# Kernel tuning notes

Hardware: AMD Instinct MI355X
Metric: run time of the kernel (lower is better)

Reference implementation:

```python
import jax, jax.numpy as jnp
import numpy as np
from jax import lax

# ---- static config (matches init_kwargs) ----
STRIDE = 16
BASE_SIZE = 16
SCALES = np.array([2., 4., 8., 16., 32.])
RATIOS = np.array([0.5, 1., 2.])
CLIP = 4.14
NMS_THRESH = 0.7
PRE_NMS = 6000
POST_NMS = 300
MIN_SIZE = 16.0


def _whctrs(a):
    w = a[2] - a[0] + 1.0
    h = a[3] - a[1] + 1.0
    return w, h, a[0] + 0.5 * (w - 1.0), a[1] + 0.5 * (h - 1.0)


def _mkanchors(ws, hs, xc, yc):
    return np.stack([xc - 0.5 * (ws - 1.0), yc - 0.5 * (hs - 1.0),
                     xc + 0.5 * (ws - 1.0), yc + 0.5 * (hs - 1.0)], axis=1)


def _base_anchors():
    ba = np.array([1.0, 1.0, BASE_SIZE, BASE_SIZE]) - 1.0
    w, h, xc, yc = _whctrs(ba)
    size = w * h
    ws = np.round(np.sqrt(size / RATIOS))
    hs = np.round(ws * RATIOS)
    ra = _mkanchors(ws, hs, xc, yc)
    out = []
    for i in range(ra.shape[0]):
        w, h, xc, yc = _whctrs(ra[i])
        out.append(_mkanchors(w * SCALES, h * SCALES, xc, yc))
    return np.concatenate(out, axis=0)  # (A,4), A = len(ratios)*len(scales)


def _grid_anchors(Hf, Wf):
    ba = _base_anchors()                       # (A,4)
    sx, sy = np.meshgrid(np.arange(Wf) * STRIDE, np.arange(Hf) * STRIDE)
    shifts = np.stack([sx, sy, sx, sy], axis=-1)          # (Hf,Wf,4)
    anch = shifts[:, :, None, :] + ba[None, None, :, :]    # (Hf,Wf,A,4)
    return jnp.asarray(anch.reshape(1, -1, 4), dtype=jnp.float32)


def _decode_clip(anchors, deltas, img_h, img_w):
    # NormalizedBoxCenterDecoder (stds=1) + clip to image
    aw = anchors[..., 2] - anchors[..., 0]
    ah = anchors[..., 3] - anchors[..., 1]
    ax = anchors[..., 0] + 0.5 * aw
    ay = anchors[..., 1] + 0.5 * ah
    dx, dy, dw, dh = deltas[..., 0], deltas[..., 1], deltas[..., 2], deltas[..., 3]
    ox = dx * aw + ax
    oy = dy * ah + ay
    ow = jnp.exp(jnp.minimum(dw, CLIP)) * aw * 0.5
    oh = jnp.exp(jnp.minimum(dh, CLIP)) * ah * 0.5
    x1 = jnp.clip(ox - ow, 0.0, img_w - 1.0)
    y1 = jnp.clip(oy - oh, 0.0, img_h - 1.0)
    x2 = jnp.clip(ox + ow, 0.0, img_w - 1.0)
    y2 = jnp.clip(oy + oh, 0.0, img_h - 1.0)
    return jnp.stack([x1, y1, x2, y2], axis=-1)


def _nms_single(scores, boxes):
    # scores (N,), boxes (N,4). Greedy NMS, force_suppress, sorted by score desc.
    order = jnp.argsort(-scores)[:PRE_NMS]
    s = scores[order]
    b = boxes[order]
    x1, y1, x2, y2 = b[:, 0], b[:, 1], b[:, 2], b[:, 3]
    area = (x2 - x1) * (y2 - y1)
    iw = jnp.maximum(jnp.minimum(x2[:, None], x2[None, :]) - jnp.maximum(x1[:, None], x1[None, :]), 0.0)
    ih = jnp.maximum(jnp.minimum(y2[:, None], y2[None, :]) - jnp.maximum(y1[:, None], y1[None, :]), 0.0)
    inter = iw * ih
    iou = inter / (area[:, None] + area[None, :] - inter + 1e-12)  # (PRE,PRE)

    supp0 = s < 0.0  # invalid entries (score set to -1 by min_size filter)

    def body(supp, i):
        keep = jnp.logical_not(supp[i])
        new = jnp.where(keep, jnp.logical_or(supp, iou[i] > NMS_THRESH), supp)
        new = new.at[i].set(supp[i])  # never self-suppress
        return new, None

    supp, _ = lax.scan(body, supp0, jnp.arange(PRE_NMS))
    kept = jnp.logical_not(supp)
    perm = jnp.argsort(jnp.where(kept, 0, 1), stable=True)  # kept boxes first, order preserved
    out_s = jnp.where(kept[perm], s[perm], -1.0)
    out_b = jnp.where(kept[perm][:, None], b[perm], -1.0)
    return out_s[:POST_NMS, None], out_b[:POST_NMS]


def _forward(img, x, conv_w, conv_b, score_w, score_b, loc_w, loc_b):
    B, _, Hf, Wf = x.shape
    img_h, img_w = float(img.shape[2]), float(img.shape[3])
    anchors = _grid_anchors(Hf, Wf)  # (1, Hf*Wf*A, 4)

    # conv1 3x3 pad 1 + ReLU
    h = lax.conv_general_dilated(x, conv_w, (1, 1), [(1, 1), (1, 1)],
                                 dimension_numbers=('NCHW', 'OIHW', 'NCHW'))
    h = jax.nn.relu(h + conv_b[None, :, None, None])

    A = score_w.shape[0]
    raw_scores = jnp.einsum('bchw,oc->bhwo', h, score_w.reshape(A, -1)) + score_b
    raw_scores = raw_scores.reshape(B, -1, 1)                       # (B,N,1)
    raw_boxes = jnp.einsum('bchw,oc->bhwo', h, loc_w.reshape(4 * A, -1)) + loc_b
    raw_boxes = raw_boxes.reshape(B, -1, 4)                         # (B,N,4)

    rpn_scores = jax.nn.sigmoid(raw_scores)

    roi = _decode_clip(anchors, raw_boxes, img_h, img_w)            # (B,N,4)
    width = roi[..., 2] - roi[..., 0]
    height = roi[..., 3] - roi[..., 1]
    invalid = jnp.logical_or(width < MIN_SIZE, height < MIN_SIZE)   # (B,N)
    score = jnp.where(invalid[..., None], -1.0, rpn_scores)         # (B,N,1)
    roi = jnp.where(invalid[..., None], -1.0, roi)

    out_s, out_b = jax.vmap(_nms_single)(score[..., 0], roi)        # (B,300,1),(B,300,4)
    return jnp.concatenate([out_s, out_b], axis=-1)                 # (B,300,5)


def setup_inputs() -> dict:
    key = jax.random.key(0)
    ks = jax.random.split(key, 8)
    img = jax.random.normal(ks[0], (1, 3, 1024, 1024), jnp.float32)
    x = jax.random.normal(ks[1], (1, 1024, 64, 64), jnp.float32)
    conv_w = jax.random.normal(ks[2], (1024, 1024, 3, 3), jnp.float32) * 0.01
    conv_b = jnp.zeros((1024,), jnp.float32)
    score_w = jax.random.normal(ks[3], (15, 1024, 1, 1), jnp.float32) * 0.01
    score_b = jnp.zeros((15,), jnp.float32)
    loc_w = jax.random.normal(ks[4], (60, 1024, 1, 1), jnp.float32) * 0.002
    loc_b = jnp.zeros((60,), jnp.float32)
    return {"img": img, "x": x, "conv_w": conv_w, "conv_b": conv_b,
            "score_w": score_w, "score_b": score_b, "loc_w": loc_w, "loc_b": loc_b}


def reference(img, x, conv_w, conv_b, score_w, score_b, loc_w, loc_b):
    return _forward(img, x, conv_w, conv_b, score_w, score_b, loc_w, loc_b)
```

## Files before the change

kernel.cpp:

```cpp
#include <hip/hip_runtime.h>

typedef unsigned int uint;
typedef unsigned short ushort;
typedef unsigned long long u64;

typedef __attribute__((ext_vector_type(8))) short short8;
typedef __attribute__((ext_vector_type(4))) float floatx4;

__device__ inline ushort bf16rne(float v) {
  uint b = __float_as_uint(v);
  uint r = (b + 0x7fffu + ((b >> 16) & 1u)) >> 16;
  return (ushort)r;
}

__device__ inline void gl_lds16(const void* g, void* l) {
  __builtin_amdgcn_global_load_lds(
      (const __attribute__((address_space(1))) unsigned int*)g,
      (__attribute__((address_space(3))) unsigned int*)l, 16, 0, 0);
}

__global__ __launch_bounds__(256) void prep_x(const float* __restrict__ x,
                                              ushort* __restrict__ xh,
                                              ushort* __restrict__ xl) {
  __shared__ float tile[64 * 65];
  int ci0 = blockIdx.x * 64, y = blockIdx.y, t = threadIdx.x;
#pragma unroll
  for (int it = 0; it < 16; ++it) {
    int L = t + 256 * it;
    int cl = L >> 6, xx = L & 63;
    tile[cl * 65 + xx] = x[(size_t)(ci0 + cl) * 4096 + y * 64 + xx];
  }
  __syncthreads();
#pragma unroll
  for (int it = 0; it < 16; ++it) {
    int L = t + 256 * it;
    int xx = L >> 6, cl = L & 63;
    float v = tile[cl * 65 + xx];
    ushort h2 = bf16rne(v);
    float hf = __uint_as_float((uint)h2 << 16);
    ushort l2 = bf16rne(v - hf);
    size_t oi = ((size_t)((y + 1) * 66 + (xx + 1))) * 1024 + ci0 + cl;
    xh[oi] = h2;
    xl[oi] = l2;
  }
}

__global__ __launch_bounds__(256) void prep_w(const float* __restrict__ w,
                                              ushort* __restrict__ wh,
                                              ushort* __restrict__ wl) {
  __shared__ float tile[2304];
  int co = blockIdx.x, ci0 = blockIdx.y * 256, t = threadIdx.x;
  const float* src = w + ((size_t)co * 1024 + ci0) * 9;
  for (int i = t; i < 2304; i += 256) tile[i] = src[i];
  __syncthreads();
  int ci = ci0 + t;
#pragma unroll
  for (int off = 0; off < 9; ++off) {
    float v = tile[t * 9 + off];
    ushort h2 = bf16rne(v);
    float hf = __uint_as_float((uint)h2 << 16);
    ushort l2 = bf16rne(v - hf);
    size_t oi = ((size_t)off << 20) | ((size_t)co << 10) | (size_t)ci;
    wh[oi] = h2;
    wl[oi] = l2;
  }
}

__global__ __launch_bounds__(256) void prep_head(
    const float* __restrict__ score_w, const float* __restrict__ loc_w,
    const float* __restrict__ score_b, const float* __restrict__ loc_b,
    ushort* __restrict__ wh, ushort* __restrict__ wl, float* __restrict__ bh) {
  int idx = blockIdx.x * 256 + threadIdx.x;
  int o = idx >> 10, ci = idx & 1023;
  float v = 0.f;
  if (o < 15) v = score_w[o * 1024 + ci];
  else if (o < 75) v = loc_w[(o - 15) * 1024 + ci];
  ushort h2 = bf16rne(v);
  float hf = __uint_as_float((uint)h2 << 16);
  wh[idx] = h2;
  wl[idx] = bf16rne(v - hf);
  if (idx < 128) bh[idx] = (idx < 15) ? score_b[idx] : ((idx < 75) ? loc_b[idx - 15] : 0.f);
}

template <int IM2COL>
__global__ __launch_bounds__(256, 1) void gemm_bf16x3(
    const ushort* __restrict__ Ahi, const ushort* __restrict__ Alo,
    const ushort* __restrict__ Bhi, const ushort* __restrict__ Blo,
    const float* __restrict__ bias, int nChunks, float* __restrict__ outRaw,
    ushort* __restrict__ outHi, ushort* __restrict__ outLo) {
  __shared__ ushort sm[2 * 4 * 128 * 32];
  const int t = threadIdx.x;
  const int m0 = blockIdx.x * 128;
  const int n0 = blockIdx.y * 128;

  auto stage = [&](int kc, int bufIdx) {
    char* lds = (char*)sm + bufIdx * 32768;
    int off = 0, cc = 0, oy = 0, ox = 0;
    if (IM2COL) {
      off = kc >> 5;
      cc = (kc & 31) << 5;
      oy = off / 3;
      ox = off - 3 * oy;
    }
#pragma unroll
    for (int q = 0; q < 2; ++q) {
      int L = t + 256 * q, row = L >> 2, seg = L & 3;
      size_t aoff, boff;
      if (IM2COL) {
        int m = m0 + row, y = m >> 6, xq = m & 63;
        aoff = ((size_t)((y + oy) * 66 + (xq + ox)) * 1024 + (size_t)cc) * 2 + seg * 16;
        boff = (((size_t)off << 20) + ((size_t)(n0 + row) << 10) + (size_t)cc) * 2 + seg * 16;
      } else {
        aoff = (((size_t)(m0 + row) << 10) + (size_t)kc * 32) * 2 + seg * 16;
        boff = (((size_t)(n0 + row) << 10) + (size_t)kc * 32) * 2 + seg * 16;
      }
      int dst = L * 16;
      gl_lds16((const char*)Ahi + aoff, lds + dst);
      gl_lds16((const char*)Alo + aoff, lds + 8192 + dst);
      gl_lds16((const char*)Bhi + boff, lds + 16384 + dst);
      gl_lds16((const char*)Blo + boff, lds + 24576 + dst);
    }
  };

  const int lane = t & 63, wv = t >> 6;
  const int wm = (wv & 1) * 64, wn = (wv >> 1) * 64;
  const int arow = wm + (lane & 15);
  const int brow = wn + (lane & 15);
  const int ko = (lane >> 4) * 8;

  floatx4 acc[4][4];
#pragma unroll
  for (int i = 0; i < 4; ++i)
#pragma unroll
    for (int j = 0; j < 4; ++j) acc[i][j] = (floatx4){0.f, 0.f, 0.f, 0.f};

  stage(0, 0);
  for (int kc = 0; kc < nChunks; ++kc) {
    __syncthreads();
    if (kc + 1 < nChunks) stage(kc + 1, (kc + 1) & 1);
    const ushort* sb = sm + (kc & 1) * 16384;
    const ushort* sAh = sb;
    const ushort* sAl = sb + 4096;
    const ushort* sBh = sb + 8192;
    const ushort* sBl = sb + 12288;
    short8 ah[4], al[4], bh2[4], bl2[4];
#pragma unroll
    for (int i = 0; i < 4; ++i) {
      ah[i] = *(const short8*)(sAh + (arow + 16 * i) * 32 + ko);
      al[i] = *(const short8*)(sAl + (arow + 16 * i) * 32 + ko);
      bh2[i] = *(const short8*)(sBh + (brow + 16 * i) * 32 + ko);
      bl2[i] = *(const short8*)(sBl + (brow + 16 * i) * 32 + ko);
    }
#pragma unroll
    for (int i = 0; i < 4; ++i)
#pragma unroll
      for (int j = 0; j < 4; ++j) {
        acc[i][j] = __builtin_amdgcn_mfma_f32_16x16x32_bf16(ah[i], bh2[j], acc[i][j], 0, 0, 0);
        acc[i][j] = __builtin_amdgcn_mfma_f32_16x16x32_bf16(ah[i], bl2[j], acc[i][j], 0, 0, 0);
        acc[i][j] = __builtin_amdgcn_mfma_f32_16x16x32_bf16(al[i], bh2[j], acc[i][j], 0, 0, 0);
      }
  }

#pragma unroll
  for (int i = 0; i < 4; ++i)
#pragma unroll
    for (int j = 0; j < 4; ++j) {
      int nn = n0 + wn + 16 * j + (lane & 15);
      float bv = bias[nn];
#pragma unroll
      for (int r = 0; r < 4; ++r) {
        int mm = m0 + wm + 16 * i + (lane >> 4) * 4 + r;
        float v = acc[i][j][r] + bv;
        if (IM2COL) {
          v = fmaxf(v, 0.f);
          ushort h2 = bf16rne(v);
          float hf = __uint_as_float((uint)h2 << 16);
          ushort l2 = bf16rne(v - hf);
          outHi[(size_t)mm * 1024 + nn] = h2;
          outLo[(size_t)mm * 1024 + nn] = l2;
        } else {
          outRaw[(size_t)mm * 128 + nn] = v;
        }
      }
    }
}

__global__ __launch_bounds__(256) void decode_k(const float* __restrict__ raw,
                                                float* __restrict__ scores,
                                                float4* __restrict__ boxes,
                                                uint* __restrict__ key32,
                                                uint* __restrict__ hist) {
  int i = blockIdx.x * 256 + threadIdx.x;
  int m = i / 15, a = i - m * 15;
  int y = m >> 6, x = m & 63;
  const float* rp = raw + (size_t)m * 128;
  float logit = rp[a];
  float dx = rp[15 + 4 * a], dy = rp[16 + 4 * a];
  float dw = rp[17 + 4 * a], dh = rp[18 + 4 * a];
  int rr = a / 5, ss = a - rr * 5;
  float sc5 = (float)(2 << ss);
  float W = ((rr == 0) ? 23.f : (rr == 1) ? 16.f : 11.f) * sc5;
  float H = ((rr == 0) ? 12.f : (rr == 1) ? 16.f : 22.f) * sc5;
  float aw = W - 1.f, ah = H - 1.f;
  float ax = x * 16.f + 7.5f, ay = y * 16.f + 7.5f;
  float ox = dx * aw + ax, oyc = dy * ah + ay;
  float ow = expf(fminf(dw, 4.14f)) * aw * 0.5f;
  float oh = expf(fminf(dh, 4.14f)) * ah * 0.5f;
  float x1 = fminf(fmaxf(ox - ow, 0.f), 1023.f);
  float y1 = fminf(fmaxf(oyc - oh, 0.f), 1023.f);
  float x2 = fminf(fmaxf(ox + ow, 0.f), 1023.f);
  float y2 = fminf(fmaxf(oyc + oh, 0.f), 1023.f);
  bool inval = ((x2 - x1) < 16.f) || ((y2 - y1) < 16.f);
  float sc = inval ? -1.f : (1.f / (1.f + expf(-logit)));
  scores[i] = sc;
  boxes[i] = inval ? make_float4(-1.f, -1.f, -1.f, -1.f) : make_float4(x1, y1, x2, y2);
  uint kb = __float_as_uint(sc);
  uint key = (kb & 0x80000000u) ? ~kb : (kb | 0x80000000u);
  key32[i] = key;
  atomicAdd(&hist[key >> 16], 1u);
}

__global__ __launch_bounds__(256) void find_t16(const uint* __restrict__ hist,
                                                uint* __restrict__ selT) {
  __shared__ uint ps[256];
  __shared__ int segS;
  int t = threadIdx.x;
  uint s = 0;
  const uint* hp = hist + t * 256;
  for (int i = 0; i < 256; ++i) s += hp[i];
  ps[t] = s;
  __syncthreads();
  for (int d = 1; d < 256; d <<= 1) {
    uint v = ps[t] + ((t + d < 256) ? ps[t + d] : 0u);
    __syncthreads();
    ps[t] = v;
    __syncthreads();
  }
  if (ps[t] >= 6000u && (t == 255 || ps[t + 1] < 6000u)) segS = t;
  __syncthreads();
  int sg = segS;
  uint base = (sg == 255) ? 0u : ps[sg + 1];
  uint h2 = hist[sg * 256 + t];
  __syncthreads();
  ps[t] = h2;
  __syncthreads();
  for (int d = 1; d < 256; d <<= 1) {
    uint v = ps[t] + ((t + d < 256) ? ps[t + d] : 0u);
    __syncthreads();
    ps[t] = v;
    __syncthreads();
  }
  if (base + ps[t] >= 6000u && (t == 255 || base + ps[t + 1] < 6000u))
    *selT = (uint)(sg * 256 + t);
}

__global__ __launch_bounds__(256) void gather_k(const uint* __restrict__ key32,
                                                const uint* __restrict__ selT,
                                                uint* __restrict__ cnt,
                                                u64* __restrict__ cand) {
  int i = blockIdx.x * 256 + threadIdx.x;
  uint T = *selT;
  uint k = key32[i];
  if ((k >> 16) >= T) {
    uint pos = atomicAdd(cnt, 1u);
    if (pos < 8192) cand[pos] = ((u64)k << 32) | (u64)(~(uint)i);
  }
}

__global__ __launch_bounds__(1024) void sort_gather(
    const u64* __restrict__ cand, const uint* __restrict__ cnt,
    const float* __restrict__ scores, const float4* __restrict__ boxes,
    float* __restrict__ sortedS, float4* __restrict__ sortedB) {
  extern __shared__ u64 sk[];
  int t = threadIdx.x;
  int C = (int)*cnt;
  if (C > 8192) C = 8192;
  for (int j = t; j < 8192; j += 1024) sk[j] = (j < C) ? cand[j] : 0ull;
  __syncthreads();
  for (int k = 2; k <= 8192; k <<= 1) {
    for (int j2 = k >> 1; j2 > 0; j2 >>= 1) {
      for (int p = t; p < 4096; p += 1024) {
        int i = ((p & ~(j2 - 1)) << 1) | (p & (j2 - 1));
        int ix = i | j2;
        u64 a = sk[i], b = sk[ix];
        bool ddir = (i & k) != 0;
        if ((a < b) != ddir) { sk[i] = b; sk[ix] = a; }
      }
      __syncthreads();
    }
  }
  for (int j = t; j < 6016; j += 1024) {
    if (j < 6000) {
      u64 key = sk[j];
      uint idx = ~(uint)(key & 0xffffffffu);
      sortedS[j] = scores[idx];
      sortedB[j] = boxes[idx];
    } else {
      sortedS[j] = -1.f;
      sortedB[j] = make_float4(0.f, 0.f, 0.f, 0.f);
    }
  }
}

__global__ __launch_bounds__(64) void iou_mask(const float4* __restrict__ boxes,
                                               u64* __restrict__ mask) {
  __shared__ float cx1[64], cy1[64], cx2[64], cy2[64], car[64];
  int bi = blockIdx.x, bj = blockIdx.y, t = threadIdx.x;
  float4 cb = boxes[bj * 64 + t];
  cx1[t] = cb.x; cy1[t] = cb.y; cx2[t] = cb.z; cy2[t] = cb.w;
  car[t] = (cb.z - cb.x) * (cb.w - cb.y);
  __syncthreads();
  int r = bi * 64 + t;
  float4 rb = boxes[r];
  float ra = (rb.z - rb.x) * (rb.w - rb.y);
  u64 wd = 0;
#pragma unroll 8
  for (int j = 0; j < 64; ++j) {
    float iw = fmaxf(fminf(rb.z, cx2[j]) - fmaxf(rb.x, cx1[j]), 0.f);
    float ih = fmaxf(fminf(rb.w, cy2[j]) - fmaxf(rb.y, cy1[j]), 0.f);
    float inter = iw * ih;
    float iou = inter / (ra + car[j] - inter + 1e-12f);
    if (iou > 0.7f && r != bj * 64 + j) wd |= (1ull << j);
  }
  mask[(size_t)r * 128 + bj] = wd;
}

__global__ __launch_bounds__(64) void nms_scan(const u64* __restrict__ mask,
                                               const float* __restrict__ sortedS,
                                               const float4* __restrict__ sortedB,
                                               float* __restrict__ out) {
  __shared__ int klist[300];
  int lane = threadIdx.x;
  u64 Sx = 0, Sy = 0;
  for (int w2 = 0; w2 < 94; ++w2) {
    bool neg = sortedS[w2 * 64 + lane] < 0.f;
    u64 m2 = __ballot(neg);
    if ((w2 >> 1) == lane) { if (w2 & 1) Sy = m2; else Sx = m2; }
  }
  int count = 0;
  for (int w2 = 0; w2 < 94; ++w2) {
    u64 cur = __shfl((w2 & 1) ? Sy : Sx, w2 >> 1);
    u64 rem = ~cur;
    if (w2 == 93) rem &= (1ull << 48) - 1;
    while (rem) {
      int b = __builtin_ctzll(rem);
      int i = w2 * 64 + b;
      if (lane == 0) klist[count] = i;
      count++;
      if (count == 300) goto done;
      const ulonglong2* rp = (const ulonglong2*)(mask + (size_t)i * 128);
      ulonglong2 rv = rp[lane];
      Sx |= rv.x;
      Sy |= rv.y;
      u64 cur2 = __shfl((w2 & 1) ? Sy : Sx, w2 >> 1);
      rem &= ~cur2;
      rem &= (b == 63) ? 0ull : (~0ull << (b + 1));
    }
  }
done:
  __syncthreads();
  for (int j = lane; j < 300; j += 64) {
    float s;
    float4 bb;
    if (j < count) {
      int i = klist[j];
      s = sortedS[i];
      bb = sortedB[i];
    } else {
      s = -1.f;
      bb = make_float4(-1.f, -1.f, -1.f, -1.f);
    }
    out[j * 5 + 0] = s;
    out[j * 5 + 1] = bb.x;
    out[j * 5 + 2] = bb.y;
    out[j * 5 + 3] = bb.z;
    out[j * 5 + 4] = bb.w;
  }
}

constexpr size_t O_XH = 0;
constexpr size_t O_XL = 8921088;
constexpr size_t O_WTH = 17842176;
constexpr size_t O_WTL = 36716544;
constexpr size_t O_HH = 55590912;
constexpr size_t O_HL = 63979520;
constexpr size_t O_WHH = 72368128;
constexpr size_t O_WHL = 72630272;
constexpr size_t O_BHD = 72892416;
constexpr size_t O_SC = 72892928;
constexpr size_t O_BX = 73138688;
constexpr size_t O_KEY = 74121728;
constexpr size_t O_HIST = 74367488;
constexpr size_t O_CNT = 74629632;
constexpr size_t O_CAND = 74629888;
constexpr size_t O_SELT = 74695424;
constexpr size_t O_SS = 74695680;
constexpr size_t O_SB = 74719744;
constexpr size_t O_RAW = 0;
constexpr size_t O_MASK = 17842176;

extern "C" void kernel_launch(void* const* d_in, const int* in_sizes, int n_in,
                              void* d_out, int out_size, void* d_ws,
                              size_t ws_size, hipStream_t stream) {
  (void)in_sizes; (void)n_in; (void)out_size; (void)ws_size;
  const float* x = (const float*)d_in[1];
  const float* conv_w = (const float*)d_in[2];
  const float* conv_b = (const float*)d_in[3];
  const float* score_w = (const float*)d_in[4];
  const float* score_b = (const float*)d_in[5];
  const float* loc_w = (const float*)d_in[6];
  const float* loc_b = (const float*)d_in[7];
  float* out = (float*)d_out;
  char* ws = (char*)d_ws;

  ushort* xh = (ushort*)(ws + O_XH);
  ushort* xl = (ushort*)(ws + O_XL);
  ushort* wTh = (ushort*)(ws + O_WTH);
  ushort* wTl = (ushort*)(ws + O_WTL);
  ushort* hh = (ushort*)(ws + O_HH);
  ushort* hl = (ushort*)(ws + O_HL);
  ushort* wHh = (ushort*)(ws + O_WHH);
  ushort* wHl = (ushort*)(ws + O_WHL);
  float* biasH = (float*)(ws + O_BHD);
  float* raw = (float*)(ws + O_RAW);
  float* scores = (float*)(ws + O_SC);
  float4* boxes = (float4*)(ws + O_BX);
  uint* key32 = (uint*)(ws + O_KEY);
  uint* hist = (uint*)(ws + O_HIST);
  uint* cnt = (uint*)(ws + O_CNT);
  u64* cand = (u64*)(ws + O_CAND);
  uint* selT = (uint*)(ws + O_SELT);
  float* sortedS = (float*)(ws + O_SS);
  float4* sortedB = (float4*)(ws + O_SB);
  u64* mask = (u64*)(ws + O_MASK);

  hipMemsetAsync(ws + O_XH, 0, 2 * 8921088, stream);
  hipMemsetAsync(ws + O_HIST, 0, 262144 + 256, stream);

  prep_x<<<dim3(16, 64), 256, 0, stream>>>(x, xh, xl);
  prep_w<<<dim3(1024, 4), 256, 0, stream>>>(conv_w, wTh, wTl);
  prep_head<<<512, 256, 0, stream>>>(score_w, loc_w, score_b, loc_b, wHh, wHl, biasH);

  gemm_bf16x3<1><<<dim3(32, 8), 256, 0, stream>>>(xh, xl, wTh, wTl, conv_b, 288,
                                                  nullptr, hh, hl);
  gemm_bf16x3<0><<<dim3(32, 1), 256, 0, stream>>>(hh, hl, wHh, wHl, biasH, 32,
                                                  raw, nullptr, nullptr);

  decode_k<<<240, 256, 0, stream>>>(raw, scores, boxes, key32, hist);
  find_t16<<<1, 256, 0, stream>>>(hist, selT);
  gather_k<<<240, 256, 0, stream>>>(key32, selT, cnt, cand);
  sort_gather<<<1, 1024, 65536, stream>>>(cand, cnt, scores, boxes, sortedS, sortedB);
  iou_mask<<<dim3(94, 94), 64, 0, stream>>>(sortedB, mask);
  nms_scan<<<1, 64, 0, stream>>>(mask, sortedS, sortedB, out);
}
```

Before: 744.1 us.

## Template GEMM on N tile width and switch LDS layout to segment-major

The bf16x3 GEMM is templated on the N tile size. The main 3x3 conv GEMM now uses 64-wide N tiles, giving 512 blocks instead of 256 so the mi355x's CUs are better filled. The LDS staging layout also changes from row-major (row, seg) to segment-major (seg, row), which changes the bank access pattern of the short8 fragment reads and likely reduces bank conflicts. Narrower tiles lower per-block arithmetic intensity and increase A-tile reloads from global memory.

```diff
diff --git a/kernel.cpp b/kernel.cpp
--- a/kernel.cpp
+++ b/kernel.cpp
@@ -82,79 +82,101 @@
   if (idx < 128) bh[idx] = (idx < 15) ? score_b[idx] : ((idx < 75) ? loc_b[idx - 15] : 0.f);
 }
 
-template <int IM2COL>
+template <int IM2COL, int BN>
 __global__ __launch_bounds__(256, 1) void gemm_bf16x3(
     const ushort* __restrict__ Ahi, const ushort* __restrict__ Alo,
     const ushort* __restrict__ Bhi, const ushort* __restrict__ Blo,
     const float* __restrict__ bias, int nChunks, float* __restrict__ outRaw,
     ushort* __restrict__ outHi, ushort* __restrict__ outLo) {
-  __shared__ ushort sm[2 * 4 * 128 * 32];
+  constexpr int ASEC = 128 * 32;
+  constexpr int BSEC = BN * 32;
+  constexpr int BUFU = 2 * ASEC + 2 * BSEC;
+  constexpr int NJ = BN / 32;
+  __shared__ ushort sm[2 * BUFU];
   const int t = threadIdx.x;
   const int m0 = blockIdx.x * 128;
-  const int n0 = blockIdx.y * 128;
-
-  auto stage = [&](int kc, int bufIdx) {
-    char* lds = (char*)sm + bufIdx * 32768;
+  const int n0 = blockIdx.y * BN;
+
+  auto stage = [&](int c, int bufIdx) {
+    ushort* secAh = sm + bufIdx * BUFU;
+    ushort* secAl = secAh + ASEC;
+    ushort* secBh = secAl + ASEC;
+    ushort* secBl = secBh + BSEC;
     int off = 0, cc = 0, oy = 0, ox = 0;
     if (IM2COL) {
-      off = kc >> 5;
-      cc = (kc & 31) << 5;
+      off = c >> 5;
+      cc = (c & 31) << 5;
       oy = off / 3;
       ox = off - 3 * oy;
     }
 #pragma unroll
     for (int q = 0; q < 2; ++q) {
-      int L = t + 256 * q, row = L >> 2, seg = L & 3;
-      size_t aoff, boff;
+      int L = t + 256 * q;
+      int row = L & 127, seg = L >> 7;
+      size_t aoff;
       if (IM2COL) {
         int m = m0 + row, y = m >> 6, xq = m & 63;
         aoff = ((size_t)((y + oy) * 66 + (xq + ox)) * 1024 + (size_t)cc) * 2 + seg * 16;
+      } else {
+        aoff = (((size_t)(m0 + row) << 10) + (size_t)c * 32) * 2 + seg * 16;
+      }
+      gl_lds16((const char*)Ahi + aoff, (char*)secAh + L * 16);
+      gl_lds16((const char*)Alo + aoff, (char*)secAl + L * 16);
+    }
+#pragma unroll
+    for (int q = 0; q < BN / 64; ++q) {
+      int L = t + 256 * q;
+      int row = L & (BN - 1), seg = L / BN;
+      size_t boff;
+      if (IM2COL) {
         boff = (((size_t)off << 20) + ((size_t)(n0 + row) << 10) + (size_t)cc) * 2 + seg * 16;
       } else {
-        aoff = (((size_t)(m0 + row) << 10) + (size_t)kc * 32) * 2 + seg * 16;
-        boff = (((size_t)(n0 + row) << 10) + (size_t)kc * 32) * 2 + seg * 16;
+        boff = (((size_t)(n0 + row) << 10) + (size_t)c * 32) * 2 + seg * 16;
       }
-      int dst = L * 16;
-      gl_lds16((const char*)Ahi + aoff, lds + dst);
-      gl_lds16((const char*)Alo + aoff, lds + 8192 + dst);
-      gl_lds16((const char*)Bhi + boff, lds + 16384 + dst);
-      gl_lds16((const char*)Blo + boff, lds + 24576 + dst);
+      gl_lds16((const char*)Bhi + boff, (char*)secBh + L * 16);
+      gl_lds16((const char*)Blo + boff, (char*)secBl + L * 16);
     }
   };
 
   const int lane = t & 63, wv = t >> 6;
-  const int wm = (wv & 1) * 64, wn = (wv >> 1) * 64;
-  const int arow = wm + (lane & 15);
-  const int brow = wn + (lane & 15);
-  const int ko = (lane >> 4) * 8;
-
-  floatx4 acc[4][4];
+  const int wm = (wv & 1) * 64, wn = (wv >> 1) * (BN / 2);
+  const int rA = wm + (lane & 15);
+  const int rB = wn + (lane & 15);
+  const int segA = (lane >> 4) * 2048;
+  const int segB = (lane >> 4) * (BN * 16);
+
+  floatx4 acc[4][NJ];
 #pragma unroll
   for (int i = 0; i < 4; ++i)
 #pragma unroll
-    for (int j = 0; j < 4; ++j) acc[i][j] = (floatx4){0.f, 0.f, 0.f, 0.f};
+    for (int j = 0; j < NJ; ++j) acc[i][j] = (floatx4){0.f, 0.f, 0.f, 0.f};
 
   stage(0, 0);
   for (int kc = 0; kc < nChunks; ++kc) {
     __syncthreads();
     if (kc + 1 < nChunks) stage(kc + 1, (kc + 1) & 1);
-    const ushort* sb = sm + (kc & 1) * 16384;
-    const ushort* sAh = sb;
-    const ushort* sAl = sb + 4096;
-    const ushort* sBh = sb + 8192;
-    const ushort* sBl = sb + 12288;
-    short8 ah[4], al[4], bh2[4], bl2[4];
+    const ushort* sb = sm + (kc & 1) * BUFU;
+    const char* cAh = (const char*)sb;
+    const char* cAl = (const char*)(sb + ASEC);
+    const char* cBh = (const char*)(sb + 2 * ASEC);
+    const char* cBl = (const char*)(sb + 2 * ASEC + BSEC);
+    short8 ah[4], al[4], bh2[NJ], bl2[NJ];
 #pragma unroll
     for (int i = 0; i < 4; ++i) {
-      ah[i] = *(const short8*)(sAh + (arow + 16 * i) * 32 + ko);
-      al[i] = *(const short8*)(sAl + (arow + 16 * i) * 32 + ko);
-      bh2[i] = *(const short8*)(sBh + (brow + 16 * i) * 32 + ko);
-      bl2[i] = *(const short8*)(sBl + (brow + 16 * i) * 32 + ko);
+      int pa = segA + (rA + 16 * i) * 16;
+      ah[i] = *(const short8*)(cAh + pa);
+      al[i] = *(const short8*)(cAl + pa);
+    }
+#pragma unroll
+    for (int j = 0; j < NJ; ++j) {
+      int pb = segB + (rB + 16 * j) * 16;
+      bh2[j] = *(const short8*)(cBh + pb);
+      bl2[j] = *(const short8*)(cBl + pb);
     }
 #pragma unroll
     for (int i = 0; i < 4; ++i)
 #pragma unroll
-      for (int j = 0; j < 4; ++j) {
+      for (int j = 0; j < NJ; ++j) {
         acc[i][j] = __builtin_amdgcn_mfma_f32_16x16x32_bf16(ah[i], bh2[j], acc[i][j], 0, 0, 0);
         acc[i][j] = __builtin_amdgcn_mfma_f32_16x16x32_bf16(ah[i], bl2[j], acc[i][j], 0, 0, 0);
         acc[i][j] = __builtin_amdgcn_mfma_f32_16x16x32_bf16(al[i], bh2[j], acc[i][j], 0, 0, 0);
@@ -164,7 +186,7 @@
 #pragma unroll
   for (int i = 0; i < 4; ++i)
 #pragma unroll
-    for (int j = 0; j < 4; ++j) {
+    for (int j = 0; j < NJ; ++j) {
       int nn = n0 + wn + 16 * j + (lane & 15);
       float bv = bias[nn];
 #pragma unroll
@@ -441,10 +463,10 @@
   prep_w<<<dim3(1024, 4), 256, 0, stream>>>(conv_w, wTh, wTl);
   prep_head<<<512, 256, 0, stream>>>(score_w, loc_w, score_b, loc_b, wHh, wHl, biasH);
 
-  gemm_bf16x3<1><<<dim3(32, 8), 256, 0, stream>>>(xh, xl, wTh, wTl, conv_b, 288,
-                                                  nullptr, hh, hl);
-  gemm_bf16x3<0><<<dim3(32, 1), 256, 0, stream>>>(hh, hl, wHh, wHl, biasH, 32,
-                                                  raw, nullptr, nullptr);
+  gemm_bf16x3<1, 64><<<dim3(32, 16), 256, 0, stream>>>(xh, xl, wTh, wTl, conv_b,
+                                                       288, nullptr, hh, hl);
+  gemm_bf16x3<0, 128><<<dim3(32, 1), 256, 0, stream>>>(hh, hl, wHh, wHl, biasH,
+                                                       32, raw, nullptr, nullptr);
 
   decode_k<<<240, 256, 0, stream>>>(raw, scores, boxes, key32, hist);
   find_t16<<<1, 256, 0, stream>>>(hist, selT);
```

Measured after the change: 947.9 us. +27.4%, slower.
